# Performance work log

Measured on AMD Instinct MI355X. Metric: run time of the kernel, lower is better.

Reference implementation:

```python
import jax, jax.numpy as jnp
import numpy as np

EMBED = 1024
HEADS = 16
HEAD_DIM = EMBED // HEADS
HIDDEN = 4096
EPS = 1e-5


def setup_inputs() -> dict:
    key = jax.random.key(0)
    ks = jax.random.split(key, 16)
    s_e = 1.0 / np.sqrt(EMBED)
    s_h = 1.0 / np.sqrt(HIDDEN)
    return {
        "x": jax.random.normal(ks[0], (8, 1024, EMBED), dtype=jnp.float32),
        "ln1_g": jnp.ones((EMBED,), jnp.float32),
        "ln1_b": jnp.zeros((EMBED,), jnp.float32),
        "ln2_g": jnp.ones((EMBED,), jnp.float32),
        "ln2_b": jnp.zeros((EMBED,), jnp.float32),
        "wq": jax.random.uniform(ks[1], (EMBED, EMBED), jnp.float32, -s_e, s_e),
        "bq": jax.random.uniform(ks[2], (EMBED,), jnp.float32, -s_e, s_e),
        "wk": jax.random.uniform(ks[3], (EMBED, EMBED), jnp.float32, -s_e, s_e),
        "bk": jax.random.uniform(ks[4], (EMBED,), jnp.float32, -s_e, s_e),
        "wv": jax.random.uniform(ks[5], (EMBED, EMBED), jnp.float32, -s_e, s_e),
        "bv": jax.random.uniform(ks[6], (EMBED,), jnp.float32, -s_e, s_e),
        "wo": jax.random.uniform(ks[7], (EMBED, EMBED), jnp.float32, -s_e, s_e),
        "bo": jax.random.uniform(ks[8], (EMBED,), jnp.float32, -s_e, s_e),
        "w1": jax.random.uniform(ks[9], (EMBED, HIDDEN), jnp.float32, -s_e, s_e),
        "b1": jax.random.uniform(ks[10], (HIDDEN,), jnp.float32, -s_e, s_e),
        "w2": jax.random.uniform(ks[11], (HIDDEN, EMBED), jnp.float32, -s_h, s_h),
        "b2": jax.random.uniform(ks[12], (EMBED,), jnp.float32, -s_h, s_h),
    }


def _layernorm(x, g, b):
    mu = jnp.mean(x, axis=-1, keepdims=True)
    var = jnp.mean((x - mu) ** 2, axis=-1, keepdims=True)
    return (x - mu) * jax.lax.rsqrt(var + EPS) * g + b


def reference(x, ln1_g, ln1_b, ln2_g, ln2_b, wq, bq, wk, bk, wv, bv, wo, bo, w1, b1, w2, b2):
    B, N, E = x.shape
    scale = HEAD_DIM ** (-0.5)
    # --- attention sublayer (pre-norm) ---
    h = _layernorm(x, ln1_g, ln1_b)
    q = (h @ wq + bq).reshape(B, N, HEADS, HEAD_DIM).transpose(0, 2, 1, 3) * scale
    k = (h @ wk + bk).reshape(B, N, HEADS, HEAD_DIM).transpose(0, 2, 1, 3)
    v = (h @ wv + bv).reshape(B, N, HEADS, HEAD_DIM).transpose(0, 2, 1, 3)
    scores = jnp.einsum("bhqd,bhkd->bhqk", q, k)
    attn = jax.nn.softmax(scores, axis=-1)
    ctx = jnp.einsum("bhqk,bhkd->bhqd", attn, v)
    ctx = ctx.transpose(0, 2, 1, 3).reshape(B, N, E)
    x = x + (ctx @ wo + bo)
    # --- FFN sublayer (pre-norm) ---
    h2 = _layernorm(x, ln2_g, ln2_b)
    ff = jax.nn.relu(h2 @ w1 + b1) @ w2 + b2
    return x + ff
```

## Files before the change

kernel.cpp:

```cpp
#include <hip/hip_runtime.h>
#include <hip/hip_bf16.h>

typedef __attribute__((ext_vector_type(4))) float f32x4;
typedef __attribute__((ext_vector_type(16))) float f32x16;
typedef __attribute__((ext_vector_type(8))) __bf16 bf16x8;
typedef __attribute__((ext_vector_type(4))) __bf16 bf16x4;
typedef __attribute__((ext_vector_type(4))) unsigned int u32x4;

static constexpr int E    = 1024;
static constexpr int TOK  = 8192;
static constexpr int HID  = 4096;

#define DEVINL __device__ __forceinline__

DEVINL void gload16(const void* g, void* l) {
  __builtin_amdgcn_global_load_lds((__attribute__((address_space(1))) void*)g,
                                   (__attribute__((address_space(3))) void*)l, 16, 0, 0);
}

#define ABAR()  asm volatile("s_barrier" ::: "memory")
#define AVM(n)  asm volatile("s_waitcnt vmcnt(" #n ")" ::: "memory")
#define ALGKM0() do { asm volatile("s_waitcnt lgkmcnt(0)" ::: "memory"); \
                      __builtin_amdgcn_sched_barrier(0); } while (0)
#define CVTPK(dst, lo, hi) asm("v_cvt_pk_bf16_f32 %0, %1, %2" : "=v"(dst) : "v"(lo), "v"(hi))
#define PLSWAP(a, b) asm("v_permlane32_swap_b32 %0, %1" : "+v"(a), "+v"(b))

template <int N> DEVINL void avm() {
  if constexpr (N == 0)      asm volatile("s_waitcnt vmcnt(0)" ::: "memory");
  else if constexpr (N == 2) asm volatile("s_waitcnt vmcnt(2)" ::: "memory");
  else if constexpr (N == 8) asm volatile("s_waitcnt vmcnt(8)" ::: "memory");
  else if constexpr (N == 9) asm volatile("s_waitcnt vmcnt(9)" ::: "memory");
  else                       asm volatile("s_waitcnt vmcnt(0)" ::: "memory");
}

__global__ __launch_bounds__(256) void wconv_kernel(const float* __restrict__ W,
                                                    __bf16* __restrict__ Wt,
                                                    int K, int N) {
  __shared__ float tile[32][33];
  const int t  = threadIdx.x;
  const long k0 = (long)blockIdx.y * 32;
  const long n0 = (long)blockIdx.x * 32;
  const int r  = t >> 3;
  const int c4 = (t & 7) * 4;
  float4 v = *(const float4*)&W[(k0 + r) * N + n0 + c4];
  tile[r][c4 + 0] = v.x; tile[r][c4 + 1] = v.y;
  tile[r][c4 + 2] = v.z; tile[r][c4 + 3] = v.w;
  __syncthreads();
  bf16x4 o;
#pragma unroll
  for (int i = 0; i < 4; ++i) o[i] = (__bf16)tile[c4 + i][r];
  *(bf16x4*)&Wt[(n0 + r) * K + k0 + c4] = o;
}

__global__ __launch_bounds__(256) void ln_kernel(const float* __restrict__ X,
                                                 const float* __restrict__ g,
                                                 const float* __restrict__ be,
                                                 __bf16* __restrict__ O) {
  const int t = threadIdx.x;
  const long row = blockIdx.x;
  float4 v = *(const float4*)&X[row * E + t * 4];
  float s  = v.x + v.y + v.z + v.w;
  float ss = v.x * v.x + v.y * v.y + v.z * v.z + v.w * v.w;
#pragma unroll
  for (int off = 32; off; off >>= 1) {
    s  += __shfl_down(s, off);
    ss += __shfl_down(ss, off);
  }
  __shared__ float red[8];
  const int w = t >> 6;
  if ((t & 63) == 0) { red[w] = s; red[4 + w] = ss; }
  __syncthreads();
  s  = red[0] + red[1] + red[2] + red[3];
  ss = red[4] + red[5] + red[6] + red[7];
  const float mean = s * (1.0f / E);
  const float var  = ss * (1.0f / E) - mean * mean;
  const float rstd = rsqrtf(var + 1e-5f);
  float4 gv = *(const float4*)&g[t * 4];
  float4 bv = *(const float4*)&be[t * 4];
  bf16x4 o;
  o[0] = (__bf16)((v.x - mean) * rstd * gv.x + bv.x);
  o[1] = (__bf16)((v.y - mean) * rstd * gv.y + bv.y);
  o[2] = (__bf16)((v.z - mean) * rstd * gv.z + bv.z);
  o[3] = (__bf16)((v.w - mean) * rstd * gv.w + bv.w);
  *(bf16x4*)&O[row * E + t * 4] = o;
}

__global__ __launch_bounds__(256) void reduce2_kernel(float* __restrict__ out,
                                                      const __bf16* __restrict__ t0,
                                                      const __bf16* __restrict__ t1,
                                                      const float* __restrict__ b2) {
  const int i = blockIdx.x * 256 + threadIdx.x;
  float4 o = ((const float4*)out)[i];
  bf16x4 a = ((const bf16x4*)t0)[i];
  bf16x4 b = ((const bf16x4*)t1)[i];
  float4 bb = ((const float4*)b2)[i & 255];
  o.x += bb.x + (float)a[0] + (float)b[0];
  o.y += bb.y + (float)a[1] + (float)b[1];
  o.z += bb.z + (float)a[2] + (float)b[2];
  o.w += bb.w + (float)a[3] + (float)b[3];
  ((float4*)out)[i] = o;
}

template <int BM_, int DEPTH, bool RELU, bool RESID, bool OUTBF, int NB>
__global__ __launch_bounds__(512, 2) void gemmk_kernel(const __bf16* __restrict__ A,
                                                       const __bf16* __restrict__ Bt,
                                                       const float* __restrict__ bias0,
                                                       const float* __restrict__ bias1,
                                                       const float* __restrict__ bias2,
                                                       const float* resid,
                                                       void* Cout, void* Cout2,
                                                       int M, int N, int K, int KLD) {
  extern __shared__ char lds[];
  constexpr int MF    = BM_ / 32;
  constexpr int ABYT  = BM_ * 64;
  constexpr int TILEB = ABYT + 16384;
  constexpr int AL    = BM_ / 128;
  constexpr int TL    = AL + 2;
  constexpr int W     = (DEPTH - 2) * TL;

  const int tid  = threadIdx.x;
  const int lane = tid & 63;
  const int l15  = lane & 15;
  const int kp   = lane >> 4;
  const int wid  = tid >> 6;
  const int wr   = wid >> 2;
  const int wc   = wid & 3;

  const int gx   = gridDim.x, gy = gridDim.y;
  const int nwg  = gx * gy * gridDim.z;
  const int flat = blockIdx.x + gx * (blockIdx.y + gy * blockIdx.z);
  const int swz  = (flat & 7) * (nwg >> 3) + (flat >> 3);
  const int bx   = swz % gx;
  const int by   = (swz / gx) % gy;
  const int bz   = swz / (gx * gy);
  const long brow = (long)by * BM_;
  const long bcol = (long)bx * 256;
  const long koff = (long)bz * K;

  const __bf16* Ab = A  + brow * KLD + koff;
  const __bf16* Bb = Bt + bcol * KLD + koff;
  void* Cdst = bz ? Cout2 : Cout;
  const int NT = K >> 5;

  auto stageA = [&](int k0, char* dst) {
#pragma unroll
    for (int i = 0; i < AL; ++i) {
      const int c = i * 512 + tid;
      const int r = c >> 2;
      const int p = (c & 3) ^ ((r >> 1) & 3);
      gload16(Ab + (long)r * KLD + k0 + p * 8, dst + c * 16);
    }
  };
  auto stageB = [&](int k0, char* dst) {
#pragma unroll
    for (int i = 0; i < 2; ++i) {
      const int c = i * 512 + tid;
      const int r = c >> 2;
      const int p = (c & 3) ^ ((r >> 1) & 3);
      gload16(Bb + (long)r * KLD + k0 + p * 8, dst + c * 16);
    }
  };

  f32x4 acc[MF][4];
  const f32x4 z4 = {0.f, 0.f, 0.f, 0.f};
#pragma unroll
  for (int m = 0; m < MF; ++m)
#pragma unroll
    for (int n = 0; n < 4; ++n) acc[m][n] = z4;

#pragma unroll
  for (int pt = 0; pt < DEPTH - 1; ++pt) {
    stageA(pt * 32, lds + pt * TILEB);
    stageB(pt * 32, lds + pt * TILEB + ABYT);
  }

  bf16x8 af[4], bfr[4];

  for (int t = 0; t < NT; ++t) {
    const int cb = t % DEPTH;
    const int sb = (t + DEPTH - 1) % DEPTH;
    const char* Ac = lds + cb * TILEB;
    const char* Bc = Ac + ABYT;
    char* An = lds + sb * TILEB;
    const int kt = (t + DEPTH - 1 < NT) ? ((t + DEPTH - 1) << 5) : 0;

    avm<W>();
    ABAR();

    if constexpr (BM_ == 256) {
#pragma unroll
      for (int m = 0; m < 4; ++m) {
        const int row = m * 32 + wr * 16 + l15;
        af[m] = *(const bf16x8*)(Ac + row * 64 + (kp ^ ((row >> 1) & 3)) * 16);
      }
#pragma unroll
      for (int n = 0; n < 4; ++n) {
        const int col = n * 64 + wc * 16 + l15;
        bfr[n] = *(const bf16x8*)(Bc + col * 64 + (kp ^ ((col >> 1) & 3)) * 16);
      }
      stageA(kt, An);
      ABAR();
      ALGKM0();
      __builtin_amdgcn_s_setprio(1);
#pragma unroll
      for (int m = 0; m < 4; ++m)
#pragma unroll
        for (int n = 0; n < 4; ++n)
          acc[m][n] = __builtin_amdgcn_mfma_f32_16x16x32_bf16(af[m], bfr[n], acc[m][n], 0, 0, 0);
      __builtin_amdgcn_s_setprio(0);
      ABAR();
#pragma unroll
      for (int m = 0; m < 4; ++m) {
        const int row = (m + 4) * 32 + wr * 16 + l15;
        af[m] = *(const bf16x8*)(Ac + row * 64 + (kp ^ ((row >> 1) & 3)) * 16);
      }
      stageB(kt, An + ABYT);
      ABAR();
      ALGKM0();
      __builtin_amdgcn_s_setprio(1);
#pragma unroll
      for (int m = 0; m < 4; ++m)
#pragma unroll
        for (int n = 0; n < 4; ++n)
          acc[m + 4][n] = __builtin_amdgcn_mfma_f32_16x16x32_bf16(af[m], bfr[n], acc[m + 4][n], 0, 0, 0);
      __builtin_amdgcn_s_setprio(0);
    } else {
#pragma unroll
      for (int m = 0; m < 4; ++m) {
        const int row = m * 32 + wr * 16 + l15;
        af[m] = *(const bf16x8*)(Ac + row * 64 + (kp ^ ((row >> 1) & 3)) * 16);
      }
#pragma unroll
      for (int n = 0; n < 4; ++n) {
        const int col = n * 64 + wc * 16 + l15;
        bfr[n] = *(const bf16x8*)(Bc + col * 64 + (kp ^ ((col >> 1) & 3)) * 16);
      }
      stageA(kt, An);
      stageB(kt, An + ABYT);
      ABAR();
      ALGKM0();
      __builtin_amdgcn_s_setprio(1);
#pragma unroll
      for (int m = 0; m < 4; ++m)
#pragma unroll
        for (int n = 0; n < 4; ++n)
          acc[m][n] = __builtin_amdgcn_mfma_f32_16x16x32_bf16(af[m], bfr[n], acc[m][n], 0, 0, 0);
      __builtin_amdgcn_s_setprio(0);
    }
  }
  avm<0>();

#pragma unroll
  for (int m = 0; m < MF; ++m) {
#pragma unroll
    for (int n = 0; n < 4; ++n) {
      const long col = bcol + n * 64 + wc * 16 + l15;
      float bb;
      if (NB == 3) {
        const float* bp = (col < 1024) ? bias0 : ((col < 2048) ? bias1 : bias2);
        bb = bp[col & 1023];
      } else if (NB == 1) {
        bb = bias0[col];
      } else {
        bb = 0.f;
      }
#pragma unroll
      for (int j = 0; j < 4; ++j) {
        const long row = brow + m * 32 + wr * 16 + (lane >> 4) * 4 + j;
        float val = acc[m][n][j] + bb;
        if (RELU) val = fmaxf(val, 0.f);
        const long idx = row * N + col;
        if (RESID) val += resid[idx];
        if (OUTBF) ((__bf16*)Cdst)[idx] = (__bf16)val;
        else       ((float*)Cdst)[idx]  = val;
      }
    }
  }
}

__global__ __launch_bounds__(256, 3) void attn_kernel(const __bf16* __restrict__ QKV,
                                                      __bf16* __restrict__ Og) {
  __shared__ __align__(16) __bf16 Qs[128 * 64];
  __shared__ __align__(16) __bf16 Ks[2][64 * 64];
  __shared__ __align__(16) __bf16 Vt[2][64 * 64];

  const int QSTR = 3072;
  const int t    = threadIdx.x;
  const int lane = t & 63;
  const int w    = t >> 6;
  const int l31  = lane & 31;
  const int h    = lane >> 5;
  const int b    = blockIdx.y >> 4;
  const int hh   = blockIdx.y & 15;
  const long row0 = (long)b * 1024 + (long)blockIdx.x * 128;
  const long kvrow0 = (long)b * 1024;
  const int colQ = hh * 64;
  const int colK = colQ + 1024;
  const int colV = colQ + 2048;

#pragma unroll
  for (int j = 0; j < 4; ++j) {
    const int c = j * 256 + t;
    const int r = c >> 3;
    const int p = (c & 7) ^ (r & 7);
    gload16(QKV + (row0 + r) * QSTR + colQ + p * 8, (char*)Qs + c * 16);
  }
#pragma unroll
  for (int j = 0; j < 2; ++j) {
    const int c = j * 256 + t;
    const int r = c >> 3;
    const int p = (c & 7) ^ (r & 7);
    gload16(QKV + (kvrow0 + r) * QSTR + colK + p * 8, (char*)Ks[0] + c * 16);
  }
  bf16x8 vv[2];
#pragma unroll
  for (int j = 0; j < 2; ++j) {
    const int c = j * 256 + t;
    const int key = c >> 3, dc = c & 7;
    vv[j] = *(const bf16x8*)(QKV + (kvrow0 + key) * QSTR + colV + dc * 8);
  }
  AVM(0);
#pragma unroll
  for (int j = 0; j < 2; ++j) {
    const int c = j * 256 + t;
    const int key = c >> 3, dc = c & 7;
#pragma unroll
    for (int e = 0; e < 8; ++e) {
      const int d = dc * 8 + e;
      *(__bf16*)((char*)Vt[0] + d * 128 + (((key >> 3) ^ dc) * 16) + (key & 7) * 2) = vv[j][e];
    }
  }
  __syncthreads();

  bf16x8 bq[4];
  {
    const int qrow = w * 32 + l31;
#pragma unroll
    for (int kk = 0; kk < 4; ++kk) {
      const int p = (kk * 2 + h) ^ (qrow & 7);
      bq[kk] = *(const bf16x8*)((const char*)Qs + qrow * 128 + p * 16);
    }
  }

  f32x16 ctx0, ctx1;
#pragma unroll
  for (int r = 0; r < 16; ++r) { ctx0[r] = 0.f; ctx1[r] = 0.f; }
  float m = -INFINITY, l = 0.f;

  for (int kb = 0; kb < 16; ++kb) {
    const int cur = kb & 1, nxt = cur ^ 1;
    const int kb1 = (kb + 1 < 16) ? kb + 1 : kb;
    const long kr1 = kvrow0 + kb1 * 64;

#pragma unroll
    for (int j = 0; j < 2; ++j) {
      const int c = j * 256 + t;
      const int key = c >> 3, dc = c & 7;
      vv[j] = *(const bf16x8*)(QKV + (kr1 + key) * QSTR + colV + dc * 8);
    }
#pragma unroll
    for (int j = 0; j < 2; ++j) {
      const int c = j * 256 + t;
      const int r = c >> 3;
      const int p = (c & 7) ^ (r & 7);
      gload16(QKV + (kr1 + r) * QSTR + colK + p * 8, (char*)Ks[nxt] + c * 16);
    }

    f32x16 s0, s1;
#pragma unroll
    for (int r = 0; r < 16; ++r) { s0[r] = 0.f; s1[r] = 0.f; }
    __builtin_amdgcn_s_setprio(1);
#pragma unroll
    for (int kk = 0; kk < 4; ++kk) {
      const int pce = kk * 2 + h;
      const int p0i = pce ^ (l31 & 7);
      bf16x8 ak0 = *(const bf16x8*)((const char*)Ks[cur] + l31 * 128 + p0i * 16);
      bf16x8 ak1 = *(const bf16x8*)((const char*)Ks[cur] + (32 + l31) * 128 + p0i * 16);
      s0 = __builtin_amdgcn_mfma_f32_32x32x16_bf16(ak0, bq[kk], s0, 0, 0, 0);
      s1 = __builtin_amdgcn_mfma_f32_32x32x16_bf16(ak1, bq[kk], s1, 0, 0, 0);
    }
    __builtin_amdgcn_s_setprio(0);

    float mx = s0[0];
#pragma unroll
    for (int r = 1; r < 16; ++r) mx = fmaxf(mx, s0[r]);
#pragma unroll
    for (int r = 0; r < 16; ++r) mx = fmaxf(mx, s1[r]);
    mx = fmaxf(mx, __shfl_xor(mx, 32));

    if (!__all(mx - m <= 64.f)) {
      const float mn = fmaxf(m, mx);
      const float corr = __expf((m - mn) * 0.125f);
      l *= corr;
#pragma unroll
      for (int r = 0; r < 16; ++r) { ctx0[r] *= corr; ctx1[r] *= corr; }
      m = mn;
    }
    f32x16 p0, p1;
    float rs = 0.f;
#pragma unroll
    for (int r = 0; r < 16; ++r) { p0[r] = __expf((s0[r] - m) * 0.125f); rs += p0[r]; }
#pragma unroll
    for (int r = 0; r < 16; ++r) { p1[r] = __expf((s1[r] - m) * 0.125f); rs += p1[r]; }
    rs += __shfl_xor(rs, 32);
    l += rs;

    AVM(2);
#pragma unroll
    for (int j = 0; j < 2; ++j) {
      const int c = j * 256 + t;
      const int key = c >> 3, dc = c & 7;
#pragma unroll
      for (int e = 0; e < 8; ++e) {
        const int d = dc * 8 + e;
        *(__bf16*)((char*)Vt[nxt] + d * 128 + (((key >> 3) ^ dc) * 16) + (key & 7) * 2) = vv[j][e];
      }
    }

    bf16x8 paf[4];
#pragma unroll
    for (int ks = 0; ks < 4; ++ks) {
      const int base = (ks & 1) * 8;
      unsigned a0, a1, b0, b1;
      if (ks < 2) {
        CVTPK(a0, p0[base + 0], p0[base + 1]);
        CVTPK(b0, p0[base + 4], p0[base + 5]);
        CVTPK(a1, p0[base + 2], p0[base + 3]);
        CVTPK(b1, p0[base + 6], p0[base + 7]);
      } else {
        CVTPK(a0, p1[base + 0], p1[base + 1]);
        CVTPK(b0, p1[base + 4], p1[base + 5]);
        CVTPK(a1, p1[base + 2], p1[base + 3]);
        CVTPK(b1, p1[base + 6], p1[base + 7]);
      }
      PLSWAP(a0, b0);
      PLSWAP(a1, b1);
      u32x4 wv4; wv4[0] = a0; wv4[1] = a1; wv4[2] = b0; wv4[3] = b1;
      paf[ks] = __builtin_bit_cast(bf16x8, wv4);
    }

    __builtin_amdgcn_s_setprio(1);
#pragma unroll
    for (int ks = 0; ks < 4; ++ks) {
      const int pce = ks * 2 + h;
      bf16x8 av0 = *(const bf16x8*)((const char*)Vt[cur] + l31 * 128 + ((pce ^ (l31 >> 3)) * 16));
      bf16x8 av1 = *(const bf16x8*)((const char*)Vt[cur] + (32 + l31) * 128 + ((pce ^ (4 + (l31 >> 3))) * 16));
      ctx0 = __builtin_amdgcn_mfma_f32_32x32x16_bf16(av0, paf[ks], ctx0, 0, 0, 0);
      ctx1 = __builtin_amdgcn_mfma_f32_32x32x16_bf16(av1, paf[ks], ctx1, 0, 0, 0);
    }
    __builtin_amdgcn_s_setprio(0);

    __syncthreads();
  }

  const float inv = 1.0f / l;
  const long orow = row0 + w * 32 + l31;
#pragma unroll
  for (int f = 0; f < 2; ++f)
#pragma unroll
    for (int tq = 0; tq < 4; ++tq) {
      bf16x4 o;
#pragma unroll
      for (int e = 0; e < 4; ++e) {
        const float v = (f ? ctx1[tq * 4 + e] : ctx0[tq * 4 + e]) * inv;
        o[e] = (__bf16)v;
      }
      const int col = colQ + f * 32 + tq * 8 + h * 4;
      *(bf16x4*)&Og[orow * E + col] = o;
    }
}

extern "C" void kernel_launch(void* const* d_in, const int* in_sizes, int n_in,
                              void* d_out, int out_size, void* d_ws, size_t ws_size,
                              hipStream_t stream) {
  const float* x     = (const float*)d_in[0];
  const float* ln1g  = (const float*)d_in[1];
  const float* ln1b  = (const float*)d_in[2];
  const float* ln2g  = (const float*)d_in[3];
  const float* ln2b  = (const float*)d_in[4];
  const float* wq    = (const float*)d_in[5];
  const float* bq    = (const float*)d_in[6];
  const float* wk    = (const float*)d_in[7];
  const float* bk    = (const float*)d_in[8];
  const float* wv    = (const float*)d_in[9];
  const float* bv    = (const float*)d_in[10];
  const float* wo    = (const float*)d_in[11];
  const float* bo    = (const float*)d_in[12];
  const float* w1    = (const float*)d_in[13];
  const float* b1    = (const float*)d_in[14];
  const float* w2    = (const float*)d_in[15];
  const float* b2    = (const float*)d_in[16];
  float* out = (float*)d_out;

  char* ws = (char*)d_ws;
  const size_t MB = 1024 * 1024;
  __bf16* Wqkv = (__bf16*)(ws + 0 * MB);
  __bf16* Wot  = (__bf16*)(ws + 6 * MB);
  __bf16* W1t  = (__bf16*)(ws + 8 * MB);
  __bf16* W2t  = (__bf16*)(ws + 16 * MB);
  __bf16* h    = (__bf16*)(ws + 24 * MB);
  __bf16* qkv  = (__bf16*)(ws + 40 * MB);
  __bf16* ctx  = (__bf16*)(ws + 88 * MB);
  __bf16* ff1  = (__bf16*)(ws + 40 * MB);
  __bf16* tmp0 = (__bf16*)(ws + 0 * MB);
  __bf16* tmp1 = (__bf16*)(ws + 24 * MB);

  const dim3 blk(256);
  const dim3 blk512(512);
  const size_t GLDS256 = 4 * (256 * 64 + 16384);
  const size_t GLDS128 = 5 * (128 * 64 + 16384);

  wconv_kernel<<<dim3(E / 32, E / 32), blk, 0, stream>>>(wq, Wqkv, E, E);
  wconv_kernel<<<dim3(E / 32, E / 32), blk, 0, stream>>>(wk, Wqkv + 1024 * 1024, E, E);
  wconv_kernel<<<dim3(E / 32, E / 32), blk, 0, stream>>>(wv, Wqkv + 2048 * 1024, E, E);
  wconv_kernel<<<dim3(E / 32, E / 32), blk, 0, stream>>>(wo, Wot, E, E);
  wconv_kernel<<<dim3(HID / 32, E / 32), blk, 0, stream>>>(w1, W1t, E, HID);
  wconv_kernel<<<dim3(E / 32, HID / 32), blk, 0, stream>>>(w2, W2t, HID, E);

  ln_kernel<<<TOK, blk, 0, stream>>>(x, ln1g, ln1b, h);

  gemmk_kernel<256, 4, false, false, true, 3><<<dim3(3072 / 256, TOK / 256), blk512, GLDS256, stream>>>(
      h, Wqkv, bq, bk, bv, nullptr, qkv, nullptr, TOK, 3072, E, E);

  attn_kernel<<<dim3(8, 128), blk, 0, stream>>>(qkv, ctx);

  gemmk_kernel<128, 5, false, true, false, 1><<<dim3(E / 256, TOK / 128), blk512, GLDS128, stream>>>(
      ctx, Wot, bo, nullptr, nullptr, x, out, nullptr, TOK, E, E, E);

  ln_kernel<<<TOK, blk, 0, stream>>>(out, ln2g, ln2b, h);

  gemmk_kernel<256, 4, true, false, true, 1><<<dim3(HID / 256, TOK / 256), blk512, GLDS256, stream>>>(
      h, W1t, b1, nullptr, nullptr, nullptr, ff1, nullptr, TOK, HID, E, E);

  gemmk_kernel<256, 4, false, false, true, 0><<<dim3(E / 256, TOK / 256, 2), blk512, GLDS256, stream>>>(
      ff1, W2t, nullptr, nullptr, nullptr, nullptr, tmp0, tmp1, TOK, E, HID / 2, HID);

  reduce2_kernel<<<TOK * E / 1024, blk, 0, stream>>>(out, tmp0, tmp1, b2);
}
```

Before: 364.8 us.

## Add 256x256 GEMM kernel with 64-wide K double buffer and four-phase schedule

Adds a new GEMM kernel for the 256x256-tile cases (QKV, FFN1, FFN2 split-K). It uses a 64-deep K step with two LDS buffers (128 KB), an XOR swizzle over 8 chunks and a four-quadrant ping-pong schedule that interleaves global-to-LDS staging with MFMA quadrants. It also remaps workgroups across 8 groups via a flat swizzle. The goal is fewer barriers per K and better overlap of loads with MFMA. The cost is 128 KB of LDS per block, which likely limits occupancy to one block per CU despite launch bounds of 2, plus a tighter vmcnt-based pipeline that is easy to get subtly wrong.

```diff
diff --git a/kernel.cpp b/kernel.cpp
--- a/kernel.cpp
+++ b/kernel.cpp
@@ -28,6 +28,7 @@
 template <int N> DEVINL void avm() {
   if constexpr (N == 0)      asm volatile("s_waitcnt vmcnt(0)" ::: "memory");
   else if constexpr (N == 2) asm volatile("s_waitcnt vmcnt(2)" ::: "memory");
+  else if constexpr (N == 6) asm volatile("s_waitcnt vmcnt(6)" ::: "memory");
   else if constexpr (N == 8) asm volatile("s_waitcnt vmcnt(8)" ::: "memory");
   else if constexpr (N == 9) asm volatile("s_waitcnt vmcnt(9)" ::: "memory");
   else                       asm volatile("s_waitcnt vmcnt(0)" ::: "memory");
@@ -101,6 +102,164 @@
   ((float4*)out)[i] = o;
 }
 
+template <bool RELU, bool RESID, bool OUTBF, int NB>
+__global__ __launch_bounds__(512, 2) void gemm8p_kernel(const __bf16* __restrict__ A,
+                                                        const __bf16* __restrict__ Bt,
+                                                        const float* __restrict__ bias0,
+                                                        const float* __restrict__ bias1,
+                                                        const float* __restrict__ bias2,
+                                                        const float* resid,
+                                                        void* Cout, void* Cout2,
+                                                        int M, int N, int K, int KLD) {
+  extern __shared__ char lds[];
+  const int tid  = threadIdx.x;
+  const int lane = tid & 63;
+  const int l15  = lane & 15;
+  const int kp   = lane >> 4;
+  const int wid  = tid >> 6;
+  const int wr   = wid >> 2;
+  const int wc   = wid & 3;
+
+  const int gx   = gridDim.x, gy = gridDim.y;
+  const int nwg  = gx * gy * gridDim.z;
+  const int flat = blockIdx.x + gx * (blockIdx.y + gy * blockIdx.z);
+  const int swz  = (flat & 7) * (nwg >> 3) + (flat >> 3);
+  const int bx   = swz % gx;
+  const int by   = (swz / gx) % gy;
+  const int bz   = swz / (gx * gy);
+  const long brow = (long)by * 256;
+  const long bcol = (long)bx * 256;
+  const long koff = (long)bz * K;
+
+  const __bf16* Ab = A  + brow * KLD + koff;
+  const __bf16* Bb = Bt + bcol * KLD + koff;
+  void* Cdst = bz ? Cout2 : Cout;
+  const int NT = K >> 6;
+
+  auto stageU = [&](const __bf16* Gb, int rc0, int k0, int dstOff) {
+#pragma unroll
+    for (int i = 0; i < 2; ++i) {
+      const int c = i * 512 + tid;
+      const int r = c >> 3;
+      const int p = (c & 7) ^ (r & 7);
+      gload16(Gb + (long)(rc0 + r) * KLD + k0 + p * 8, lds + dstOff + c * 16);
+    }
+  };
+
+  f32x4 acc[8][4];
+  const f32x4 z4 = {0.f, 0.f, 0.f, 0.f};
+#pragma unroll
+  for (int m = 0; m < 8; ++m)
+#pragma unroll
+    for (int n = 0; n < 4; ++n) acc[m][n] = z4;
+
+  bf16x8 af[4][2], bh0[2][2], bh1[2][2];
+
+  auto readA = [&](int off) {
+#pragma unroll
+    for (int mm = 0; mm < 4; ++mm)
+#pragma unroll
+      for (int kk = 0; kk < 2; ++kk) {
+        const int lr = mm * 32 + wr * 16 + l15;
+        const int p  = ((kk << 2) + kp) ^ (lr & 7);
+        af[mm][kk] = *(const bf16x8*)(lds + off + lr * 128 + p * 16);
+      }
+  };
+  auto readB = [&](int off, bf16x8 (*bf)[2]) {
+#pragma unroll
+    for (int nn = 0; nn < 2; ++nn)
+#pragma unroll
+      for (int kk = 0; kk < 2; ++kk) {
+        const int lc = nn * 64 + wc * 16 + l15;
+        const int p  = ((kk << 2) + kp) ^ (lc & 7);
+        bf[nn][kk] = *(const bf16x8*)(lds + off + lc * 128 + p * 16);
+      }
+  };
+  auto quad = [&](int mb, int nb, bf16x8 (*bf)[2]) {
+    __builtin_amdgcn_s_setprio(1);
+#pragma unroll
+    for (int mm = 0; mm < 4; ++mm)
+#pragma unroll
+      for (int nn = 0; nn < 2; ++nn) {
+        f32x4 a = acc[mb + mm][nb + nn];
+        a = __builtin_amdgcn_mfma_f32_16x16x32_bf16(af[mm][0], bf[nn][0], a, 0, 0, 0);
+        a = __builtin_amdgcn_mfma_f32_16x16x32_bf16(af[mm][1], bf[nn][1], a, 0, 0, 0);
+        acc[mb + mm][nb + nn] = a;
+      }
+    __builtin_amdgcn_s_setprio(0);
+  };
+
+  stageU(Ab, 0,   0, 0);
+  stageU(Bb, 0,   0, 32768);
+  stageU(Bb, 128, 0, 49152);
+  stageU(Ab, 128, 0, 16384);
+  stageU(Ab, 0,   64, 65536 + 0);
+  stageU(Bb, 0,   64, 65536 + 32768);
+  stageU(Bb, 128, 64, 65536 + 49152);
+  avm<6>();
+  ABAR();
+
+  for (int t = 0; t < NT; ++t) {
+    const int cb  = (t & 1) ? 65536 : 0;
+    const int nb1 = cb ^ 65536;
+    const int k1 = (t + 1 < NT) ? ((t + 1) << 6) : 0;
+    const int k2 = (t + 2 < NT) ? ((t + 2) << 6) : 0;
+
+    readA(cb + 0);
+    readB(cb + 32768, bh0);
+    stageU(Ab, 128, k1, nb1 + 16384);
+    ABAR(); ALGKM0();
+    quad(0, 0, bh0);
+    ABAR();
+
+    readB(cb + 49152, bh1);
+    stageU(Ab, 0, k2, cb + 0);
+    ABAR(); ALGKM0();
+    quad(0, 2, bh1);
+    ABAR();
+
+    readA(cb + 16384);
+    stageU(Bb, 0, k2, cb + 32768);
+    ABAR(); ALGKM0();
+    quad(4, 0, bh0);
+    ABAR();
+
+    stageU(Bb, 128, k2, cb + 49152);
+    avm<6>();
+    ABAR();
+    quad(4, 2, bh1);
+    ABAR();
+  }
+  avm<0>();
+
+#pragma unroll
+  for (int m = 0; m < 8; ++m) {
+#pragma unroll
+    for (int n = 0; n < 4; ++n) {
+      const long col = bcol + n * 64 + wc * 16 + l15;
+      float bb;
+      if (NB == 3) {
+        const float* bp = (col < 1024) ? bias0 : ((col < 2048) ? bias1 : bias2);
+        bb = bp[col & 1023];
+      } else if (NB == 1) {
+        bb = bias0[col];
+      } else {
+        bb = 0.f;
+      }
+#pragma unroll
+      for (int j = 0; j < 4; ++j) {
+        const long row = brow + m * 32 + wr * 16 + (lane >> 4) * 4 + j;
+        float val = acc[m][n][j] + bb;
+        if (RELU) val = fmaxf(val, 0.f);
+        const long idx = row * N + col;
+        if (RESID) val += resid[idx];
+        if (OUTBF) ((__bf16*)Cdst)[idx] = (__bf16)val;
+        else       ((float*)Cdst)[idx]  = val;
+      }
+    }
+  }
+}
+
 template <int BM_, int DEPTH, bool RELU, bool RESID, bool OUTBF, int NB>
 __global__ __launch_bounds__(512, 2) void gemmk_kernel(const __bf16* __restrict__ A,
                                                        const __bf16* __restrict__ Bt,
@@ -187,66 +346,26 @@
     avm<W>();
     ABAR();
 
-    if constexpr (BM_ == 256) {
-#pragma unroll
-      for (int m = 0; m < 4; ++m) {
-        const int row = m * 32 + wr * 16 + l15;
-        af[m] = *(const bf16x8*)(Ac + row * 64 + (kp ^ ((row >> 1) & 3)) * 16);
-      }
-#pragma unroll
-      for (int n = 0; n < 4; ++n) {
-        const int col = n * 64 + wc * 16 + l15;
-        bfr[n] = *(const bf16x8*)(Bc + col * 64 + (kp ^ ((col >> 1) & 3)) * 16);
-      }
-      stageA(kt, An);
-      ABAR();
-      ALGKM0();
-      __builtin_amdgcn_s_setprio(1);
-#pragma unroll
-      for (int m = 0; m < 4; ++m)
-#pragma unroll
-        for (int n = 0; n < 4; ++n)
-          acc[m][n] = __builtin_amdgcn_mfma_f32_16x16x32_bf16(af[m], bfr[n], acc[m][n], 0, 0, 0);
-      __builtin_amdgcn_s_setprio(0);
-      ABAR();
-#pragma unroll
-      for (int m = 0; m < 4; ++m) {
-        const int row = (m + 4) * 32 + wr * 16 + l15;
-        af[m] = *(const bf16x8*)(Ac + row * 64 + (kp ^ ((row >> 1) & 3)) * 16);
-      }
-      stageB(kt, An + ABYT);
-      ABAR();
-      ALGKM0();
-      __builtin_amdgcn_s_setprio(1);
-#pragma unroll
-      for (int m = 0; m < 4; ++m)
-#pragma unroll
-        for (int n = 0; n < 4; ++n)
-          acc[m + 4][n] = __builtin_amdgcn_mfma_f32_16x16x32_bf16(af[m], bfr[n], acc[m + 4][n], 0, 0, 0);
-      __builtin_amdgcn_s_setprio(0);
-    } else {
-#pragma unroll
-      for (int m = 0; m < 4; ++m) {
-        const int row = m * 32 + wr * 16 + l15;
-        af[m] = *(const bf16x8*)(Ac + row * 64 + (kp ^ ((row >> 1) & 3)) * 16);
-      }
-#pragma unroll
-      for (int n = 0; n < 4; ++n) {
-        const int col = n * 64 + wc * 16 + l15;
-        bfr[n] = *(const bf16x8*)(Bc + col * 64 + (kp ^ ((col >> 1) & 3)) * 16);
-      }
-      stageA(kt, An);
-      stageB(kt, An + ABYT);
-      ABAR();
-      ALGKM0();
-      __builtin_amdgcn_s_setprio(1);
-#pragma unroll
-      for (int m = 0; m < 4; ++m)
-#pragma unroll
-        for (int n = 0; n < 4; ++n)
-          acc[m][n] = __builtin_amdgcn_mfma_f32_16x16x32_bf16(af[m], bfr[n], acc[m][n], 0, 0, 0);
-      __builtin_amdgcn_s_setprio(0);
-    }
+#pragma unroll
+    for (int m = 0; m < 4; ++m) {
+      const int row = m * 32 + wr * 16 + l15;
+      af[m] = *(const bf16x8*)(Ac + row * 64 + (kp ^ ((row >> 1) & 3)) * 16);
+    }
+#pragma unroll
+    for (int n = 0; n < 4; ++n) {
+      const int col = n * 64 + wc * 16 + l15;
+      bfr[n] = *(const bf16x8*)(Bc + col * 64 + (kp ^ ((col >> 1) & 3)) * 16);
+    }
+    stageA(kt, An);
+    stageB(kt, An + ABYT);
+    ABAR(); ALGKM0();
+    __builtin_amdgcn_s_setprio(1);
+#pragma unroll
+    for (int m = 0; m < 4; ++m)
+#pragma unroll
+      for (int n = 0; n < 4; ++n)
+        acc[m][n] = __builtin_amdgcn_mfma_f32_16x16x32_bf16(af[m], bfr[n], acc[m][n], 0, 0, 0);
+    __builtin_amdgcn_s_setprio(0);
   }
   avm<0>();
 
@@ -507,7 +626,7 @@
 
   const dim3 blk(256);
   const dim3 blk512(512);
-  const size_t GLDS256 = 4 * (256 * 64 + 16384);
+  const size_t GLDS8P  = 131072;
   const size_t GLDS128 = 5 * (128 * 64 + 16384);
 
   wconv_kernel<<<dim3(E / 32, E / 32), blk, 0, stream>>>(wq, Wqkv, E, E);
@@ -519,7 +638,7 @@
 
   ln_kernel<<<TOK, blk, 0, stream>>>(x, ln1g, ln1b, h);
 
-  gemmk_kernel<256, 4, false, false, true, 3><<<dim3(3072 / 256, TOK / 256), blk512, GLDS256, stream>>>(
+  gemm8p_kernel<false, false, true, 3><<<dim3(3072 / 256, TOK / 256), blk512, GLDS8P, stream>>>(
       h, Wqkv, bq, bk, bv, nullptr, qkv, nullptr, TOK, 3072, E, E);
 
   attn_kernel<<<dim3(8, 128), blk, 0, stream>>>(qkv, ctx);
@@ -529,10 +648,10 @@
 
   ln_kernel<<<TOK, blk, 0, stream>>>(out, ln2g, ln2b, h);
 
-  gemmk_kernel<256, 4, true, false, true, 1><<<dim3(HID / 256, TOK / 256), blk512, GLDS256, stream>>>(
+  gemm8p_kernel<true, false, true, 1><<<dim3(HID / 256, TOK / 256), blk512, GLDS8P, stream>>>(
       h, W1t, b1, nullptr, nullptr, nullptr, ff1, nullptr, TOK, HID, E, E);
 
-  gemmk_kernel<256, 4, false, false, true, 0><<<dim3(E / 256, TOK / 256, 2), blk512, GLDS256, stream>>>(
+  gemm8p_kernel<false, false, true, 0><<<dim3(E / 256, TOK / 256, 2), blk512, GLDS8P, stream>>>(
       ff1, W2t, nullptr, nullptr, nullptr, nullptr, tmp0, tmp1, TOK, E, HID / 2, HID);
 
   reduce2_kernel<<<TOK * E / 1024, blk, 0, stream>>>(out, tmp0, tmp1, b2);
```

Result: no change. 358.5 us (-1.7%).
